# Kernel optimization log

Hardware: AMD Instinct MI355X
Metric: run time of the kernel (lower is better)

The kernel has to match this reference:

```python
import jax, jax.numpy as jnp
import numpy as np


def _hd_mask(a, n):
    """Vectorized equivalent of cal_ImageMap: overlapping window-sum ratio,
    overlap-added and normalized by coverage count.
    Windows are h x w = (H//4, W//4) with stride (h//2, w//2); since the
    stride is exactly half a window, every window is a 2x2 group of
    non-overlapping (h//2, w//2) base blocks."""
    B, C, H, W = a.shape
    h, w = H // 4, W // 4            # window size (original: width,height = H//4,W//4)
    sh, sw = h // 2, w // 2          # stride = half window
    ni, nj = H // sh, W // sw

    sub = jnp.abs(n - a)             # |Image_clear - Image_hazy|
    # per-base-block sums: [B,C,ni,nj]
    blk = sub.reshape(B, C, ni, sh, nj, sw).sum(axis=(3, 5))
    diff = blk.sum(axis=(2, 3))      # total per-image abs diff, [B,C]

    # window sums = 2x2 sums of base blocks -> [B,C,ni-1,nj-1]
    ws = blk[:, :, :-1, :-1] + blk[:, :, 1:, :-1] + blk[:, :, :-1, 1:] + blk[:, :, 1:, 1:]
    wv = ws / diff[:, :, None, None]  # per-window coefficient

    # overlap-add window values back onto the base-block grid [B,C,ni,nj]
    def pad4(x, di, dj):
        return jnp.pad(x, ((0, 0), (0, 0), (di, 1 - di), (dj, 1 - dj)))
    mask_blk = pad4(wv, 0, 0) + pad4(wv, 1, 0) + pad4(wv, 0, 1) + pad4(wv, 1, 1)

    # coverage count (map_coeff), identical overlap-add of ones: [ni,nj]
    ones = jnp.ones((ni - 1, nj - 1), a.dtype)
    def pad2(x, di, dj):
        return jnp.pad(x, ((di, 1 - di), (dj, 1 - dj)))
    coeff = pad2(ones, 0, 0) + pad2(ones, 1, 0) + pad2(ones, 0, 1) + pad2(ones, 1, 1)

    mb = mask_blk / coeff            # [B,C,ni,nj]
    # upsample block values back to pixel resolution (each block is sh x sw)
    mask = jnp.broadcast_to(mb[:, :, :, None, :, None],
                            (B, C, ni, sh, nj, sw)).reshape(B, C, H, W)
    return mask


def setup_inputs() -> dict:
    key = jax.random.key(0)
    ka, kp, kn = jax.random.split(key, 3)
    shape = (16, 3, 512, 512)
    return {
        "a": jax.random.normal(ka, shape, dtype=jnp.float32),
        "p": jax.random.normal(kp, shape, dtype=jnp.float32),
        "n": jax.random.normal(kn, shape, dtype=jnp.float32),
    }


def reference(a, p, n):
    mask = _hd_mask(a, n)
    # ablation=False path: loss = L1(mask*a, mask*p), mean reduction
    return jnp.mean(jnp.abs(mask * a - mask * p))
```

## Files before the change

kernel.cpp:

```cpp
#include <hip/hip_runtime.h>

#define WW 512
#define IMG_F 262144
#define NWG 3072
#define TOTAL_PIX 12582912.0f

__global__ __launch_bounds__(256) void hd_block_sums(
    const float* __restrict__ a, const float* __restrict__ p,
    const float* __restrict__ n, float2* __restrict__ blk)
{
    const int gb  = blockIdx.x;
    const int bc  = gb >> 6;
    const int blkid = gb & 63;
    const int bi = blkid >> 3, bj = blkid & 7;
    const int tid = threadIdx.x;

    const size_t idx0 = (size_t)bc * IMG_F
                      + (size_t)(bi * 64 + (tid >> 4)) * WW
                      + (size_t)(bj * 64 + ((tid & 15) << 2));
    const float4* pa = (const float4*)(a + idx0);
    const float4* pp = (const float4*)(p + idx0);
    const float4* pn = (const float4*)(n + idx0);

    float4 va0 = pa[0], va1 = pa[2048], va2 = pa[4096], va3 = pa[6144];
    float4 vn0 = pn[0], vn1 = pn[2048], vn2 = pn[4096], vn3 = pn[6144];
    float4 vp0 = pp[0], vp1 = pp[2048], vp2 = pp[4096], vp3 = pp[6144];

    float s1, s2;
    s1  = fabsf(vn0.x - va0.x) + fabsf(vn0.y - va0.y) + fabsf(vn0.z - va0.z) + fabsf(vn0.w - va0.w);
    s1 += fabsf(vn1.x - va1.x) + fabsf(vn1.y - va1.y) + fabsf(vn1.z - va1.z) + fabsf(vn1.w - va1.w);
    s1 += fabsf(vn2.x - va2.x) + fabsf(vn2.y - va2.y) + fabsf(vn2.z - va2.z) + fabsf(vn2.w - va2.w);
    s1 += fabsf(vn3.x - va3.x) + fabsf(vn3.y - va3.y) + fabsf(vn3.z - va3.z) + fabsf(vn3.w - va3.w);
    s2  = fabsf(va0.x - vp0.x) + fabsf(va0.y - vp0.y) + fabsf(va0.z - vp0.z) + fabsf(va0.w - vp0.w);
    s2 += fabsf(va1.x - vp1.x) + fabsf(va1.y - vp1.y) + fabsf(va1.z - vp1.z) + fabsf(va1.w - vp1.w);
    s2 += fabsf(va2.x - vp2.x) + fabsf(va2.y - vp2.y) + fabsf(va2.z - vp2.z) + fabsf(va2.w - vp2.w);
    s2 += fabsf(va3.x - vp3.x) + fabsf(va3.y - vp3.y) + fabsf(va3.z - vp3.z) + fabsf(va3.w - vp3.w);

    #pragma unroll
    for (int off = 32; off > 0; off >>= 1) {
        s1 += __shfl_xor(s1, off, 64);
        s2 += __shfl_xor(s2, off, 64);
    }
    __shared__ float r1[4], r2[4];
    const int wave = tid >> 6, lane = tid & 63;
    if (lane == 0) { r1[wave] = s1; r2[wave] = s2; }
    __syncthreads();
    if (tid == 0)
        blk[gb] = make_float2(r1[0] + r1[1] + r1[2] + r1[3],
                              r2[0] + r2[1] + r2[2] + r2[3]);
}

__global__ __launch_bounds__(1024) void hd_finalize(
    const float2* __restrict__ blk, float* __restrict__ out)
{
    const int tid  = threadIdx.x;
    const int w    = tid >> 6;
    const int lane = tid & 63;
    const int i = lane >> 3, j = lane & 7;
    __shared__ float partial[16];

    float2 q0 = blk[(w     ) * 64 + lane];
    float2 q1 = blk[(w + 16) * 64 + lane];
    float2 q2 = blk[(w + 32) * 64 + lane];

    float acc = 0.f;
    #pragma unroll
    for (int it = 0; it < 3; ++it) {
        float b  = (it == 0) ? q0.x : (it == 1) ? q1.x : q2.x;
        float bp = (it == 0) ? q0.y : (it == 1) ? q1.y : q2.y;
        float d = b;
        #pragma unroll
        for (int off = 32; off > 0; off >>= 1) d += __shfl_xor(d, off, 64);
        float b_r  = __shfl(b, lane + 8, 64);
        float b_c  = __shfl(b, lane + 1, 64);
        float b_rc = __shfl(b, lane + 9, 64);
        float wv = (i < 7 && j < 7) ? (b + b_r + b_c + b_rc) / d : 0.f;
        float wv_u  = __shfl(wv, lane - 8, 64);
        float wv_l  = __shfl(wv, lane - 1, 64);
        float wv_ul = __shfl(wv, lane - 9, 64);
        float mb = wv;
        if (i > 0)          mb += wv_u;
        if (j > 0)          mb += wv_l;
        if (i > 0 && j > 0) mb += wv_ul;
        const int ci = (i == 0 || i == 7) ? 1 : 2;
        const int cj = (j == 0 || j == 7) ? 1 : 2;
        acc += (mb / (float)(ci * cj)) * bp;
    }

    #pragma unroll
    for (int off = 32; off > 0; off >>= 1) acc += __shfl_xor(acc, off, 64);
    if (lane == 0) partial[w] = acc;
    __syncthreads();
    if (tid == 0) {
        float s = 0.f;
        #pragma unroll
        for (int k = 0; k < 16; ++k) s += partial[k];
        out[0] = s / TOTAL_PIX;
    }
}

extern "C" void kernel_launch(void* const* d_in, const int* in_sizes, int n_in,
                              void* d_out, int out_size, void* d_ws, size_t ws_size,
                              hipStream_t stream) {
    const float* a = (const float*)d_in[0];
    const float* p = (const float*)d_in[1];
    const float* n = (const float*)d_in[2];
    float2* blk = (float2*)d_ws;

    hd_block_sums<<<NWG, 256, 0, stream>>>(a, p, n, blk);
    hd_finalize<<<1, 1024, 0, stream>>>(blk, (float*)d_out);
}
```

Baseline: 31.27 us.

## Read contiguous 8-row stripes per workgroup and reduce partials per block column

```diff
diff --git a/kernel.cpp b/kernel.cpp
--- a/kernel.cpp
+++ b/kernel.cpp
@@ -5,26 +5,24 @@
 #define NWG 3072
 #define TOTAL_PIX 12582912.0f
 
-__global__ __launch_bounds__(256) void hd_block_sums(
+__global__ __launch_bounds__(256) void hd_stripe_sums(
     const float* __restrict__ a, const float* __restrict__ p,
-    const float* __restrict__ n, float2* __restrict__ blk)
+    const float* __restrict__ n, float2* __restrict__ part)
 {
-    const int gb  = blockIdx.x;
-    const int bc  = gb >> 6;
-    const int blkid = gb & 63;
-    const int bi = blkid >> 3, bj = blkid & 7;
+    const int g   = blockIdx.x;
+    const int bc  = g >> 6;
+    const int s   = g & 63;
+    const int rb  = s >> 3, sub = s & 7;
     const int tid = threadIdx.x;
 
-    const size_t idx0 = (size_t)bc * IMG_F
-                      + (size_t)(bi * 64 + (tid >> 4)) * WW
-                      + (size_t)(bj * 64 + ((tid & 15) << 2));
-    const float4* pa = (const float4*)(a + idx0);
-    const float4* pp = (const float4*)(p + idx0);
-    const float4* pn = (const float4*)(n + idx0);
+    const size_t base4 = ((size_t)bc * IMG_F + (size_t)s * 4096) >> 2;
+    const float4* pa = (const float4*)a + base4 + tid;
+    const float4* pp = (const float4*)p + base4 + tid;
+    const float4* pn = (const float4*)n + base4 + tid;
 
-    float4 va0 = pa[0], va1 = pa[2048], va2 = pa[4096], va3 = pa[6144];
-    float4 vn0 = pn[0], vn1 = pn[2048], vn2 = pn[4096], vn3 = pn[6144];
-    float4 vp0 = pp[0], vp1 = pp[2048], vp2 = pp[4096], vp3 = pp[6144];
+    float4 va0 = pa[0], va1 = pa[256], va2 = pa[512], va3 = pa[768];
+    float4 vn0 = pn[0], vn1 = pn[256], vn2 = pn[512], vn3 = pn[768];
+    float4 vp0 = pp[0], vp1 = pp[256], vp2 = pp[512], vp3 = pp[768];
 
     float s1, s2;
     s1  = fabsf(vn0.x - va0.x) + fabsf(vn0.y - va0.y) + fabsf(vn0.z - va0.z) + fabsf(vn0.w - va0.w);
@@ -37,21 +35,25 @@
     s2 += fabsf(va3.x - vp3.x) + fabsf(va3.y - vp3.y) + fabsf(va3.z - vp3.z) + fabsf(va3.w - vp3.w);
 
     #pragma unroll
-    for (int off = 32; off > 0; off >>= 1) {
+    for (int off = 8; off > 0; off >>= 1) {
         s1 += __shfl_xor(s1, off, 64);
         s2 += __shfl_xor(s2, off, 64);
     }
-    __shared__ float r1[4], r2[4];
+    __shared__ float2 red[16];
     const int wave = tid >> 6, lane = tid & 63;
-    if (lane == 0) { r1[wave] = s1; r2[wave] = s2; }
+    if ((lane & 15) == 0) red[wave * 4 + (lane >> 4)] = make_float2(s1, s2);
     __syncthreads();
-    if (tid == 0)
-        blk[gb] = make_float2(r1[0] + r1[1] + r1[2] + r1[3],
-                              r2[0] + r2[1] + r2[2] + r2[3]);
+    if (tid < 8) {
+        const int cb = tid, w0 = cb >> 2, gr = cb & 3;
+        float2 x = red[w0 * 4 + gr];
+        float2 y = red[(w0 + 2) * 4 + gr];
+        part[(((bc * 8 + rb) * 8 + cb) << 3) + sub] =
+            make_float2(x.x + y.x, x.y + y.y);
+    }
 }
 
 __global__ __launch_bounds__(1024) void hd_finalize(
-    const float2* __restrict__ blk, float* __restrict__ out)
+    const float2* __restrict__ part, float* __restrict__ out)
 {
     const int tid  = threadIdx.x;
     const int w    = tid >> 6;
@@ -59,15 +61,14 @@
     const int i = lane >> 3, j = lane & 7;
     __shared__ float partial[16];
 
-    float2 q0 = blk[(w     ) * 64 + lane];
-    float2 q1 = blk[(w + 16) * 64 + lane];
-    float2 q2 = blk[(w + 32) * 64 + lane];
-
     float acc = 0.f;
     #pragma unroll
     for (int it = 0; it < 3; ++it) {
-        float b  = (it == 0) ? q0.x : (it == 1) ? q1.x : q2.x;
-        float bp = (it == 0) ? q0.y : (it == 1) ? q1.y : q2.y;
+        const int bc = w + it * 16;
+        const float4* q = (const float4*)part + ((size_t)(bc * 64 + lane) << 2);
+        float4 u0 = q[0], u1 = q[1], u2 = q[2], u3 = q[3];
+        float b  = ((u0.x + u0.z) + (u1.x + u1.z)) + ((u2.x + u2.z) + (u3.x + u3.z));
+        float bp = ((u0.y + u0.w) + (u1.y + u1.w)) + ((u2.y + u2.w) + (u3.y + u3.w));
         float d = b;
         #pragma unroll
         for (int off = 32; off > 0; off >>= 1) d += __shfl_xor(d, off, 64);
@@ -92,10 +93,10 @@
     if (lane == 0) partial[w] = acc;
     __syncthreads();
     if (tid == 0) {
-        float s = 0.f;
+        float ssum = 0.f;
         #pragma unroll
-        for (int k = 0; k < 16; ++k) s += partial[k];
-        out[0] = s / TOTAL_PIX;
+        for (int k = 0; k < 16; ++k) ssum += partial[k];
+        out[0] = ssum / TOTAL_PIX;
     }
 }
 
@@ -105,8 +106,8 @@
     const float* a = (const float*)d_in[0];
     const float* p = (const float*)d_in[1];
     const float* n = (const float*)d_in[2];
-    float2* blk = (float2*)d_ws;
+    float2* part = (float2*)d_ws;
 
-    hd_block_sums<<<NWG, 256, 0, stream>>>(a, p, n, blk);
-    hd_finalize<<<1, 1024, 0, stream>>>(blk, (float*)d_out);
+    hd_stripe_sums<<<NWG, 256, 0, stream>>>(a, p, n, part);
+    hd_finalize<<<1, 1024, 0, stream>>>(part, (float*)d_out);
 }
```

Result: no change. 31.59 us (+1.0%).
